# Kernel tuning notes

Measured on AMD Instinct MI355X. Metric: run time of the kernel, lower is better.

The kernel has to match this reference:

```python
import jax, jax.numpy as jnp
import numpy as np

B, S, DM = 2, 2048, 1024
H, HD = 16, 64  # heads, head_dims = dims // heads
SCALE = HD ** -0.5


def softmax_one(x):
    # softmax with +1 in the denominator: exp(x_i) / (1 + sum_j exp(x_j))
    # stable form: shift by m = max(max(x), 0)
    m = jnp.maximum(jnp.max(x, axis=-1, keepdims=True), 0.0)
    e = jnp.exp(x - m)
    return e / (jnp.exp(-m) + jnp.sum(e, axis=-1, keepdims=True))


def setup_inputs() -> dict:
    key = jax.random.key(0)
    ks = jax.random.split(key, 11)
    init = lambda k, shape, fan_in: jax.random.uniform(k, shape, jnp.float32, -1.0, 1.0) * (fan_in ** -0.5)
    return {
        "query": jax.random.normal(ks[0], (B, S, DM), jnp.float32),
        "key": jax.random.normal(ks[1], (B, S, DM), jnp.float32),
        "value": jax.random.normal(ks[2], (B, S, DM), jnp.float32),
        "Wq": init(ks[3], (H * HD, DM), DM), "bq": init(ks[4], (H * HD,), DM),
        "Wk": init(ks[5], (H * HD, DM), DM), "bk": init(ks[6], (H * HD,), DM),
        "Wv": init(ks[7], (H * HD, DM), DM), "bv": init(ks[8], (H * HD,), DM),
        "Wo": init(ks[9], (DM, H * HD), H * HD), "bo": init(ks[10], (DM,), H * HD),
    }


def _proj(x, W, b):
    # [B,S,DM] -> [B,H,S,HD]
    y = x @ W.T + b
    return y.reshape(B, S, H, HD).transpose(0, 2, 1, 3)


def reference(query, key, value, Wq, bq, Wk, bk, Wv, bv, Wo, bo):
    Q = _proj(query, Wq, bq)
    K = _proj(key, Wk, bk)
    V = _proj(value, Wv, bv)
    scores = jnp.einsum("bhqd,bhkd->bhqk", Q, K) * SCALE  # [B,H,S,S]
    attn = softmax_one(scores)
    out = jnp.einsum("bhqk,bhkd->bhqd", attn, V)  # [B,H,S,HD]
    out = out.transpose(0, 2, 1, 3).reshape(B, S, H * HD)
    return out @ Wo.T + bo
```

## Files before the change

### kernel.cpp

```cpp
#include <hip/hip_runtime.h>

#define B_ 2
#define S_ 2048
#define DM_ 1024
#define H_ 16
#define HD_ 64
#define SCALE_ 0.125f

typedef __bf16 bf16;
typedef __attribute__((ext_vector_type(4))) __bf16 bf16x4;
typedef __attribute__((ext_vector_type(8))) __bf16 bf16x8;
typedef __attribute__((ext_vector_type(4))) float f32x4;

#define MFMA16(a, b, c) __builtin_amdgcn_mfma_f32_16x16x32_bf16((a), (b), (c), 0, 0, 0)

__device__ __forceinline__ void async16(const bf16* g, bf16* l) {
  __builtin_amdgcn_global_load_lds(
      (const __attribute__((address_space(1))) void*)g,
      (__attribute__((address_space(3))) void*)l, 16, 0, 0);
}

__global__ __launch_bounds__(256) void convert_kernel(
    const float* __restrict__ q, const float* __restrict__ k,
    const float* __restrict__ v, const float* __restrict__ wq,
    const float* __restrict__ wk, const float* __restrict__ wv,
    const float* __restrict__ wo, bf16* __restrict__ dst) {
  size_t idx = ((size_t)blockIdx.x * 256 + threadIdx.x) * 8;
  const float* src;
  size_t off;
  if (idx < 4194304) { src = q; off = idx; }
  else if (idx < 8388608) { src = k; off = idx - 4194304; }
  else if (idx < 12582912) { src = v; off = idx - 8388608; }
  else if (idx < 13631488) { src = wq; off = idx - 12582912; }
  else if (idx < 14680064) { src = wk; off = idx - 13631488; }
  else if (idx < 15728640) { src = wv; off = idx - 14680064; }
  else { src = wo; off = idx - 15728640; }
  float4 a = *(const float4*)(src + off);
  float4 b = *(const float4*)(src + off + 4);
  bf16x8 o;
  o[0] = (bf16)a.x; o[1] = (bf16)a.y; o[2] = (bf16)a.z; o[3] = (bf16)a.w;
  o[4] = (bf16)b.x; o[5] = (bf16)b.y; o[6] = (bf16)b.z; o[7] = (bf16)b.w;
  *(bf16x8*)(dst + idx) = o;
}

template <int MODE, typename OutT>
__device__ __forceinline__ void gemm_body(const bf16* A, const bf16* W,
                                          const float* bias, OutT* C,
                                          float scale) {
  constexpr int K = 1024, N = 1024;
  __shared__ __align__(16) bf16 As[128 * 32];
  __shared__ __align__(16) bf16 Bs[128 * 32];
  const int t = threadIdx.x;
  const int lane = t & 63, wave = t >> 6;
  const int quad = lane >> 4, l16 = lane & 15;
  const int m0 = blockIdx.y * 128, n0 = blockIdx.x * 128;
  const int wm = (wave >> 1) * 64, wn = (wave & 1) * 64;

  const f32x4 zero = {0.f, 0.f, 0.f, 0.f};
  f32x4 acc[4][4];
  for (int i = 0; i < 4; i++)
    for (int j = 0; j < 4; j++) acc[i][j] = zero;

  for (int k0 = 0; k0 < K; k0 += 32) {
    for (int i = 0; i < 2; ++i) {
      int c = i * 256 + t;
      int row = c >> 2, kc = (c & 3) * 8;
      async16(A + (size_t)(m0 + row) * K + k0 + kc, As + c * 8);
      async16(W + (size_t)(n0 + row) * K + k0 + kc, Bs + c * 8);
    }
    __syncthreads();

    bf16x8 af[4], bfr[4];
    for (int mb = 0; mb < 4; mb++) {
      af[mb] = *(const bf16x8*)(As + (wm + mb * 16 + l16) * 32 + quad * 8);
      bfr[mb] = *(const bf16x8*)(Bs + (wn + mb * 16 + l16) * 32 + quad * 8);
    }
    for (int mb = 0; mb < 4; mb++)
      for (int nb = 0; nb < 4; nb++)
        acc[mb][nb] = MFMA16(af[mb], bfr[nb], acc[mb][nb]);
    __syncthreads();
  }

  if constexpr (MODE == 2) {
    __shared__ __align__(16) bf16 Ct[128 * 136];
    for (int nb = 0; nb < 4; nb++) {
      int cl = wn + nb * 16 + l16;
      float bv = bias[n0 + cl] * scale;
      for (int mb = 0; mb < 4; mb++) {
        int rowb = wm + mb * 16 + quad * 4;
        bf16x4 v;
        for (int r = 0; r < 4; r++)
          v[r] = (bf16)(acc[mb][nb][r] * scale + bv);
        *(bf16x4*)(Ct + cl * 136 + rowb) = v;
      }
    }
    __syncthreads();
    int c = t >> 1, half = t & 1;
    int colg = n0 + c;
    int hh = colg >> 6, dd = colg & 63;
    int bb = m0 >> 11, s0 = m0 & (S_ - 1);
    bf16* dst = C + (((size_t)(bb * H_ + hh)) * HD_ + dd) * S_ + s0 + half * 64;
    const bf16* srcr = Ct + c * 136 + half * 64;
    for (int j = 0; j < 8; ++j)
      *(bf16x8*)(dst + j * 8) = *(const bf16x8*)(srcr + j * 8);
  } else {
    for (int nb = 0; nb < 4; nb++) {
      int col = n0 + wn + nb * 16 + l16;
      float bv = bias[col] * scale;
      for (int mb = 0; mb < 4; mb++) {
        int rowb = m0 + wm + mb * 16 + quad * 4;
        for (int r = 0; r < 4; r++) {
          int row = rowb + r;
          float o = acc[mb][nb][r] * scale + bv;
          if (MODE == 0) {
            C[(size_t)row * N + col] = (OutT)o;
          } else {
            int bb = row >> 11, s = row & (S_ - 1);
            int h = col >> 6, d = col & 63;
            C[(((size_t)(bb * H_ + h)) * S_ + s) * HD_ + d] = (OutT)o;
          }
        }
      }
    }
  }
}

__global__ __launch_bounds__(256) void qkv_proj_kernel(
    const bf16* Xc, const float* bq, const float* bk, const float* bv,
    bf16* Qo, bf16* Ko, bf16* Vo) {
  int z = blockIdx.z;
  const bf16* A = Xc + (size_t)z * 4194304;
  const bf16* W = Xc + 12582912 + (size_t)z * 1048576;
  if (z == 0)
    gemm_body<1, bf16>(A, W, bq, Qo, SCALE_);
  else if (z == 1)
    gemm_body<1, bf16>(A, W, bk, Ko, 1.0f);
  else
    gemm_body<2, bf16>(A, W, bv, Vo, 1.0f);
}

__global__ __launch_bounds__(256) void out_proj_kernel(const bf16* A,
                                                       const bf16* W,
                                                       const float* bias,
                                                       float* C) {
  gemm_body<0, float>(A, W, bias, C, 1.0f);
}

__global__ __launch_bounds__(256) void attn_kernel(const bf16* __restrict__ Q,
                                                   const bf16* __restrict__ Kg,
                                                   const bf16* __restrict__ VTg,
                                                   bf16* __restrict__ O) {
  __shared__ __align__(16) bf16 Ks[128 * 64];
  __shared__ __align__(16) bf16 Vt[64 * 128];
  __shared__ __align__(16) bf16 Ps[4 * 32 * 136];
  const int t = threadIdx.x;
  const int lane = t & 63, wave = t >> 6;
  const int quad = lane >> 4, l16 = lane & 15;
  const int q0 = blockIdx.x * 128;
  const int h = blockIdx.y, b = blockIdx.z;
  const size_t base = ((size_t)(b * H_ + h)) * S_ * HD_;
  const bf16* Qp = Q + base;
  const bf16* Kp = Kg + base;
  const bf16* Vp = VTg + base;

  bf16x8 aq[2][2];
  for (int s = 0; s < 2; s++) {
    const bf16* qr = Qp + (size_t)(q0 + wave * 32 + s * 16 + l16) * HD_;
    aq[s][0] = *(const bf16x8*)(qr + quad * 8);
    aq[s][1] = *(const bf16x8*)(qr + 32 + quad * 8);
  }

  const f32x4 zero = {0.f, 0.f, 0.f, 0.f};
  f32x4 oc[2][4];
  for (int s = 0; s < 2; s++)
    for (int d = 0; d < 4; d++) oc[s][d] = zero;
  float rs[2] = {0.f, 0.f};

  bf16* Pw = Ps + wave * (32 * 136);

  for (int kv0 = 0; kv0 < S_; kv0 += 128) {
    for (int i = 0; i < 4; ++i) {
      int c = i * 256 + t;
      int row = c >> 3, g = c & 7;
      async16(Kp + (size_t)(kv0 + row) * HD_ + (g ^ (row & 7)) * 8, Ks + c * 8);
    }
    for (int i = 0; i < 4; ++i) {
      int c = i * 256 + t;
      int d = c >> 4, g = c & 15;
      async16(Vp + (size_t)d * S_ + kv0 + (g ^ (d & 15)) * 8, Vt + c * 8);
    }
    __syncthreads();

    f32x4 sc[2][8];
    for (int s = 0; s < 2; s++)
      for (int nb = 0; nb < 8; nb++) sc[s][nb] = zero;
    for (int ks = 0; ks < 2; ks++) {
      for (int nb = 0; nb < 8; nb++) {
        int row = nb * 16 + l16;
        int slot = (ks * 4 + quad) ^ (row & 7);
        bf16x8 kf = *(const bf16x8*)(Ks + row * 64 + slot * 8);
        sc[0][nb] = MFMA16(kf, aq[0][ks], sc[0][nb]);
        sc[1][nb] = MFMA16(kf, aq[1][ks], sc[1][nb]);
      }
    }

    for (int s = 0; s < 2; s++) {
      bf16* prow = Pw + (s * 16 + l16) * 136 + quad * 4;
      for (int nb = 0; nb < 8; nb++) {
        float p0 = __expf(sc[s][nb][0]);
        float p1 = __expf(sc[s][nb][1]);
        float p2 = __expf(sc[s][nb][2]);
        float p3 = __expf(sc[s][nb][3]);
        rs[s] += (p0 + p1) + (p2 + p3);
        bf16x4 pv = {(bf16)p0, (bf16)p1, (bf16)p2, (bf16)p3};
        *(bf16x4*)(prow + nb * 16) = pv;
      }
    }

    for (int ks = 0; ks < 4; ks++) {
      bf16x8 ap0 = *(const bf16x8*)(Pw + l16 * 136 + ks * 32 + quad * 8);
      bf16x8 ap1 = *(const bf16x8*)(Pw + (16 + l16) * 136 + ks * 32 + quad * 8);
      for (int db = 0; db < 4; db++) {
        int row = db * 16 + l16;
        int slot = (ks * 4 + quad) ^ (row & 15);
        bf16x8 vf = *(const bf16x8*)(Vt + row * 128 + slot * 8);
        oc[0][db] = MFMA16(ap0, vf, oc[0][db]);
        oc[1][db] = MFMA16(ap1, vf, oc[1][db]);
      }
    }
    __syncthreads();
  }

  for (int s = 0; s < 2; s++) {
    float rtot = rs[s];
    rtot += __shfl_xor(rtot, 16);
    rtot += __shfl_xor(rtot, 32);
    float l_all = 1.f + rtot;
    for (int r = 0; r < 4; r++) {
      float inv = 1.f / __shfl(l_all, quad * 4 + r);
      int qrow = q0 + wave * 32 + s * 16 + quad * 4 + r;
      size_t orow = ((size_t)(b * S_ + qrow) * H_ + h) * HD_;
      for (int db = 0; db < 4; db++)
        O[orow + db * 16 + l16] = (bf16)(oc[s][db][r] * inv);
    }
  }
}

extern "C" void kernel_launch(void* const* d_in, const int* in_sizes, int n_in,
                              void* d_out, int out_size, void* d_ws,
                              size_t ws_size, hipStream_t stream) {
  const float* query = (const float*)d_in[0];
  const float* key = (const float*)d_in[1];
  const float* value = (const float*)d_in[2];
  const float* bq = (const float*)d_in[4];
  const float* bk = (const float*)d_in[6];
  const float* bv = (const float*)d_in[8];
  const float* bo = (const float*)d_in[10];
  float* out = (float*)d_out;

  bf16* Xc = (bf16*)d_ws;
  bf16* Qw = Xc + 16777216;
  const size_t SZ = (size_t)B_ * H_ * S_ * HD_;
  bf16* Kw = Qw + SZ;
  bf16* Vw = Kw + SZ;
  bf16* Ow = Vw + SZ;

  convert_kernel<<<8192, 256, 0, stream>>>(query, key, value,
                                           (const float*)d_in[3],
                                           (const float*)d_in[5],
                                           (const float*)d_in[7],
                                           (const float*)d_in[9], Xc);
  qkv_proj_kernel<<<dim3(8, 32, 3), 256, 0, stream>>>(Xc, bq, bk, bv, Qw, Kw,
                                                      Vw);
  attn_kernel<<<dim3(S_ / 128, H_, B_), 256, 0, stream>>>(Qw, Kw, Vw, Ow);
  out_proj_kernel<<<dim3(8, 32), 256, 0, stream>>>(Ow, Xc + 15728640, bo, out);
}
```

Baseline: 245.3 us.

## Widen GEMM K-tile with swizzled LDS, retile out-proj, use exp2 with folded log2e

Several changes at once. The projection GEMM now loads 64-wide K tiles into XOR-swizzled shared memory, halving the number of barriers per K and reducing LDS bank conflicts. The output projection gets its own 64x128 tile kernel, launching twice as many blocks for better occupancy. The attention kernel folds log2(e) into the Q scale and uses the hardware exp2 instruction instead of __expf. Its grid is also flattened so that consecutive blocks cover different (batch, head) pairs.

```diff
diff --git a/kernel.cpp b/kernel.cpp
--- a/kernel.cpp
+++ b/kernel.cpp
@@ -5,7 +5,7 @@
 #define DM_ 1024
 #define H_ 16
 #define HD_ 64
-#define SCALE_ 0.125f
+#define QSCALE_ 0.18033688011112042f
 
 typedef __bf16 bf16;
 typedef __attribute__((ext_vector_type(4))) __bf16 bf16x4;
@@ -13,6 +13,7 @@
 typedef __attribute__((ext_vector_type(4))) float f32x4;
 
 #define MFMA16(a, b, c) __builtin_amdgcn_mfma_f32_16x16x32_bf16((a), (b), (c), 0, 0, 0)
+#define EXP2(x) __builtin_amdgcn_exp2f(x)
 
 __device__ __forceinline__ void async16(const bf16* g, bf16* l) {
   __builtin_amdgcn_global_load_lds(
@@ -43,13 +44,13 @@
   *(bf16x8*)(dst + idx) = o;
 }
 
-template <int MODE, typename OutT>
+template <int MODE>
 __device__ __forceinline__ void gemm_body(const bf16* A, const bf16* W,
-                                          const float* bias, OutT* C,
+                                          const float* bias, bf16* C,
                                           float scale) {
-  constexpr int K = 1024, N = 1024;
-  __shared__ __align__(16) bf16 As[128 * 32];
-  __shared__ __align__(16) bf16 Bs[128 * 32];
+  constexpr int K = 1024;
+  __shared__ __align__(16) bf16 As[128 * 64];
+  __shared__ __align__(16) bf16 Bs[128 * 64];
   const int t = threadIdx.x;
   const int lane = t & 63, wave = t >> 6;
   const int quad = lane >> 4, l16 = lane & 15;
@@ -61,23 +62,28 @@
   for (int i = 0; i < 4; i++)
     for (int j = 0; j < 4; j++) acc[i][j] = zero;
 
-  for (int k0 = 0; k0 < K; k0 += 32) {
-    for (int i = 0; i < 2; ++i) {
-      int c = i * 256 + t;
-      int row = c >> 2, kc = (c & 3) * 8;
-      async16(A + (size_t)(m0 + row) * K + k0 + kc, As + c * 8);
-      async16(W + (size_t)(n0 + row) * K + k0 + kc, Bs + c * 8);
-    }
-    __syncthreads();
-
-    bf16x8 af[4], bfr[4];
-    for (int mb = 0; mb < 4; mb++) {
-      af[mb] = *(const bf16x8*)(As + (wm + mb * 16 + l16) * 32 + quad * 8);
-      bfr[mb] = *(const bf16x8*)(Bs + (wn + mb * 16 + l16) * 32 + quad * 8);
-    }
-    for (int mb = 0; mb < 4; mb++)
-      for (int nb = 0; nb < 4; nb++)
-        acc[mb][nb] = MFMA16(af[mb], bfr[nb], acc[mb][nb]);
+  for (int k0 = 0; k0 < K; k0 += 64) {
+    for (int i = 0; i < 4; ++i) {
+      int c = i * 256 + t;
+      int row = c >> 3, g = c & 7;
+      int off = k0 + ((g ^ (row & 7)) * 8);
+      async16(A + (size_t)(m0 + row) * K + off, As + c * 8);
+      async16(W + (size_t)(n0 + row) * K + off, Bs + c * 8);
+    }
+    __syncthreads();
+
+    for (int ks = 0; ks < 2; ks++) {
+      bf16x8 af[4], bfr[4];
+      for (int mb = 0; mb < 4; mb++) {
+        int ra = wm + mb * 16 + l16;
+        af[mb] = *(const bf16x8*)(As + ra * 64 + ((ks * 4 + quad) ^ (ra & 7)) * 8);
+        int rb = wn + mb * 16 + l16;
+        bfr[mb] = *(const bf16x8*)(Bs + rb * 64 + ((ks * 4 + quad) ^ (rb & 7)) * 8);
+      }
+      for (int mb = 0; mb < 4; mb++)
+        for (int nb = 0; nb < 4; nb++)
+          acc[mb][nb] = MFMA16(af[mb], bfr[nb], acc[mb][nb]);
+    }
     __syncthreads();
   }
 
@@ -112,13 +118,9 @@
         for (int r = 0; r < 4; r++) {
           int row = rowb + r;
           float o = acc[mb][nb][r] * scale + bv;
-          if (MODE == 0) {
-            C[(size_t)row * N + col] = (OutT)o;
-          } else {
-            int bb = row >> 11, s = row & (S_ - 1);
-            int h = col >> 6, d = col & 63;
-            C[(((size_t)(bb * H_ + h)) * S_ + s) * HD_ + d] = (OutT)o;
-          }
+          int bb = row >> 11, s = row & (S_ - 1);
+          int h = col >> 6, d = col & 63;
+          C[(((size_t)(bb * H_ + h)) * S_ + s) * HD_ + d] = (bf16)o;
         }
       }
     }
@@ -132,18 +134,64 @@
   const bf16* A = Xc + (size_t)z * 4194304;
   const bf16* W = Xc + 12582912 + (size_t)z * 1048576;
   if (z == 0)
-    gemm_body<1, bf16>(A, W, bq, Qo, SCALE_);
+    gemm_body<1>(A, W, bq, Qo, QSCALE_);
   else if (z == 1)
-    gemm_body<1, bf16>(A, W, bk, Ko, 1.0f);
+    gemm_body<1>(A, W, bk, Ko, 1.0f);
   else
-    gemm_body<2, bf16>(A, W, bv, Vo, 1.0f);
+    gemm_body<2>(A, W, bv, Vo, 1.0f);
 }
 
 __global__ __launch_bounds__(256) void out_proj_kernel(const bf16* A,
                                                        const bf16* W,
                                                        const float* bias,
                                                        float* C) {
-  gemm_body<0, float>(A, W, bias, C, 1.0f);
+  constexpr int K = 1024, N = 1024;
+  __shared__ __align__(16) bf16 As[64 * 64];
+  __shared__ __align__(16) bf16 Bs[128 * 64];
+  const int t = threadIdx.x;
+  const int lane = t & 63, wave = t >> 6;
+  const int quad = lane >> 4, l16 = lane & 15;
+  const int m0 = blockIdx.y * 64, n0 = blockIdx.x * 128;
+
+  const f32x4 zero = {0.f, 0.f, 0.f, 0.f};
+  f32x4 acc[8];
+  for (int i = 0; i < 8; i++) acc[i] = zero;
+
+  for (int k0 = 0; k0 < K; k0 += 64) {
+    for (int i = 0; i < 2; ++i) {
+      int c = i * 256 + t;
+      int row = c >> 3, g = c & 7;
+      async16(A + (size_t)(m0 + row) * K + k0 + ((g ^ (row & 7)) * 8),
+              As + c * 8);
+    }
+    for (int i = 0; i < 4; ++i) {
+      int c = i * 256 + t;
+      int row = c >> 3, g = c & 7;
+      async16(W + (size_t)(n0 + row) * K + k0 + ((g ^ (row & 7)) * 8),
+              Bs + c * 8);
+    }
+    __syncthreads();
+
+    for (int ks = 0; ks < 2; ks++) {
+      int ra = wave * 16 + l16;
+      bf16x8 af = *(const bf16x8*)(As + ra * 64 + ((ks * 4 + quad) ^ (ra & 7)) * 8);
+      for (int nb = 0; nb < 8; nb++) {
+        int rb = nb * 16 + l16;
+        bf16x8 bfr =
+            *(const bf16x8*)(Bs + rb * 64 + ((ks * 4 + quad) ^ (rb & 7)) * 8);
+        acc[nb] = MFMA16(af, bfr, acc[nb]);
+      }
+    }
+    __syncthreads();
+  }
+
+  for (int nb = 0; nb < 8; nb++) {
+    int col = n0 + nb * 16 + l16;
+    float bv = bias[col];
+    int rowb = m0 + wave * 16 + quad * 4;
+    for (int r = 0; r < 4; r++)
+      C[(size_t)(rowb + r) * N + col] = acc[nb][r] + bv;
+  }
 }
 
 __global__ __launch_bounds__(256) void attn_kernel(const bf16* __restrict__ Q,
@@ -156,8 +204,10 @@
   const int t = threadIdx.x;
   const int lane = t & 63, wave = t >> 6;
   const int quad = lane >> 4, l16 = lane & 15;
-  const int q0 = blockIdx.x * 128;
-  const int h = blockIdx.y, b = blockIdx.z;
+  const int id = blockIdx.x;
+  const int bh = id & 31;
+  const int q0 = (id >> 5) * 128;
+  const int b = bh >> 4, h = bh & 15;
   const size_t base = ((size_t)(b * H_ + h)) * S_ * HD_;
   const bf16* Qp = Q + base;
   const bf16* Kp = Kg + base;
@@ -207,10 +257,10 @@
     for (int s = 0; s < 2; s++) {
       bf16* prow = Pw + (s * 16 + l16) * 136 + quad * 4;
       for (int nb = 0; nb < 8; nb++) {
-        float p0 = __expf(sc[s][nb][0]);
-        float p1 = __expf(sc[s][nb][1]);
-        float p2 = __expf(sc[s][nb][2]);
-        float p3 = __expf(sc[s][nb][3]);
+        float p0 = EXP2(sc[s][nb][0]);
+        float p1 = EXP2(sc[s][nb][1]);
+        float p2 = EXP2(sc[s][nb][2]);
+        float p3 = EXP2(sc[s][nb][3]);
         rs[s] += (p0 + p1) + (p2 + p3);
         bf16x4 pv = {(bf16)p0, (bf16)p1, (bf16)p2, (bf16)p3};
         *(bf16x4*)(prow + nb * 16) = pv;
@@ -272,6 +322,6 @@
                                            (const float*)d_in[9], Xc);
   qkv_proj_kernel<<<dim3(8, 32, 3), 256, 0, stream>>>(Xc, bq, bk, bv, Qw, Kw,
                                                       Vw);
-  attn_kernel<<<dim3(S_ / 128, H_, B_), 256, 0, stream>>>(Qw, Kw, Vw, Ow);
-  out_proj_kernel<<<dim3(8, 32), 256, 0, stream>>>(Ow, Xc + 15728640, bo, out);
-}
+  attn_kernel<<<512, 256, 0, stream>>>(Qw, Kw, Vw, Ow);
+  out_proj_kernel<<<dim3(8, 64), 256, 0, stream>>>(Ow, Xc + 15728640, bo, out);
+}
```

Result: no change. 249.5 us (+1.7%).
